# Kernel optimization log

Measured on AMD Instinct MI355X. Metric: run time of the kernel, lower is better.

## Reference

```python
import jax, jax.numpy as jnp
import numpy as np

B, N, P = 1, 8192, 2           # batch, volume points, global params
V, K = 5, 8                    # output variables, neighbor samples
H = HA = 256                   # basis hidden, aggregation hidden
DPOS = DGEO = DPAR = 256       # encoding dims
NOISE_INTENSITY = 50.0         # sampling radius = 1/noise_intensity


def setup_inputs() -> dict:
    key = jax.random.key(0)
    ks = jax.random.split(key, 18)
    s = 0.05
    return {
        "volume_mesh_centers": jax.random.normal(ks[0], (B, N, 3), jnp.float32),
        "encoding_g": jax.random.normal(ks[1], (B, N, DGEO), jnp.float32),
        "encoding_node": jax.random.normal(ks[2], (B, N, DPOS), jnp.float32),
        "global_params_values": jax.random.uniform(ks[3], (B, P, 1), jnp.float32, 0.5, 1.5),
        "global_params_reference": jnp.ones((B, P, 1), jnp.float32),
        # per-variable basis MLP (stacked over V)
        "Wb1": s * jax.random.normal(ks[4], (V, 3, H), jnp.float32),
        "bb1": s * jax.random.normal(ks[5], (V, H), jnp.float32),
        "Wb2": s * jax.random.normal(ks[6], (V, H, H), jnp.float32),
        "bb2": s * jax.random.normal(ks[7], (V, H), jnp.float32),
        # parameter model
        "Wp": s * jax.random.normal(ks[8], (P, DPAR), jnp.float32),
        "bp": s * jax.random.normal(ks[9], (DPAR,), jnp.float32),
        # per-variable aggregation MLP; first layer weight split by input block
        "Wa1_basis": s * jax.random.normal(ks[10], (V, H, HA), jnp.float32),
        "Wa1_node": s * jax.random.normal(ks[11], (V, DPOS, HA), jnp.float32),
        "Wa1_geo": s * jax.random.normal(ks[12], (V, DGEO, HA), jnp.float32),
        "Wa1_param": s * jax.random.normal(ks[13], (V, DPAR, HA), jnp.float32),
        "ba1": s * jax.random.normal(ks[14], (V, HA), jnp.float32),
        "Wa2": s * jax.random.normal(ks[15], (V, HA), jnp.float32),
        "ba2": s * jax.random.normal(ks[16], (V,), jnp.float32),
    }


def reference(volume_mesh_centers, encoding_g, encoding_node,
              global_params_values, global_params_reference,
              Wb1, bb1, Wb2, bb2, Wp, bp,
              Wa1_basis, Wa1_node, Wa1_geo, Wa1_param, ba1, Wa2, ba2):
    r = 1.0 / NOISE_INTENSITY
    b, n, _ = volume_mesh_centers.shape
    kd, kr = jax.random.split(jax.random.key(42))

    # sample_sphere: uniform-in-volume samples around each center.
    # NOTE: faithful to torch.rand_like(unsqueezed_center) -> per-coordinate radius.
    d = jax.random.normal(kd, (b, n, K, 3), volume_mesh_centers.dtype)
    d = d / jnp.linalg.norm(d, axis=-1, keepdims=True)
    radii = r * jax.random.uniform(kr, (b, n, K, 3), volume_mesh_centers.dtype) ** (1.0 / 3.0)
    samples = volume_mesh_centers[:, :, None, :] + d * radii
    # perturbed centers: original point first, then K neighbors -> (B,N,S,3)
    coords = jnp.concatenate([volume_mesh_centers[:, :, None, :], samples], axis=2)

    # parameter encoding: normalize by reference, expand over N (value is
    # identical for every point, so compute once per batch), then param MLP.
    ratio = (global_params_values / global_params_reference)[..., 0]  # (B,P)
    pe = jax.nn.relu(ratio @ Wp + bp)  # (B,DPAR)

    # per-variable basis MLP over all perturbed points: (B,N,S,V,H)
    h1 = jax.nn.relu(jnp.einsum('bnsc,vch->bnsvh', coords, Wb1) + bb1)
    h2 = jax.nn.relu(jnp.einsum('bnsvh,vhg->bnsvg', h1, Wb2) + bb2)

    # aggregation layer 1 = Linear(concat(basis, enc_node, enc_g, pe)).
    # Split the concat-matmul; encoding blocks are S-independent -> compute once.
    enc = (jnp.einsum('bnd,vdh->bnvh', encoding_node, Wa1_node)
           + jnp.einsum('bnd,vdh->bnvh', encoding_g, Wa1_geo)
           + jnp.einsum('bd,vdh->bvh', pe, Wa1_param)[:, None]
           + ba1)  # (B,N,V,HA)
    a1 = jax.nn.relu(jnp.einsum('bnsvg,vgh->bnsvh', h2, Wa1_basis) + enc[:, :, None])
    out = jnp.einsum('bnsvh,vh->bnsv', a1, Wa2) + ba2  # (B,N,S,V)

    # average: half weight on center prediction, half on mean of neighbors
    return 0.5 * out[:, :, 0] + 0.5 * jnp.mean(out[:, :, 1:], axis=2)  # (B,N,V)
```

## Files before the change

kernel.cpp:

```cpp
#include <hip/hip_runtime.h>

typedef unsigned int u32;
typedef unsigned short u16;
typedef short short8 __attribute__((ext_vector_type(8)));
typedef float f32x4 __attribute__((ext_vector_type(4)));
typedef u32 u32x2 __attribute__((ext_vector_type(2)));
typedef u32 u32x4 __attribute__((ext_vector_type(4)));

#define DEV static __device__ __forceinline__

__host__ __device__ constexpr u32 rotl32(u32 x, int r){ return (x << r) | (x >> (32 - r)); }
struct TF2 { u32 a, b; };

__host__ __device__ constexpr TF2 threefry2x32(u32 k0, u32 k1, u32 x0, u32 x1){
  u32 ks0 = k0, ks1 = k1, ks2 = k0 ^ k1 ^ 0x1BD11BDAu;
  x0 += ks0; x1 += ks1;
  x0 += x1; x1 = rotl32(x1,13); x1 ^= x0;
  x0 += x1; x1 = rotl32(x1,15); x1 ^= x0;
  x0 += x1; x1 = rotl32(x1,26); x1 ^= x0;
  x0 += x1; x1 = rotl32(x1, 6); x1 ^= x0;
  x0 += ks1; x1 += ks2 + 1u;
  x0 += x1; x1 = rotl32(x1,17); x1 ^= x0;
  x0 += x1; x1 = rotl32(x1,29); x1 ^= x0;
  x0 += x1; x1 = rotl32(x1,16); x1 ^= x0;
  x0 += x1; x1 = rotl32(x1,24); x1 ^= x0;
  x0 += ks2; x1 += ks0 + 2u;
  x0 += x1; x1 = rotl32(x1,13); x1 ^= x0;
  x0 += x1; x1 = rotl32(x1,15); x1 ^= x0;
  x0 += x1; x1 = rotl32(x1,26); x1 ^= x0;
  x0 += x1; x1 = rotl32(x1, 6); x1 ^= x0;
  x0 += ks0; x1 += ks1 + 3u;
  x0 += x1; x1 = rotl32(x1,17); x1 ^= x0;
  x0 += x1; x1 = rotl32(x1,29); x1 ^= x0;
  x0 += x1; x1 = rotl32(x1,16); x1 ^= x0;
  x0 += x1; x1 = rotl32(x1,24); x1 ^= x0;
  x0 += ks1; x1 += ks2 + 4u;
  x0 += x1; x1 = rotl32(x1,13); x1 ^= x0;
  x0 += x1; x1 = rotl32(x1,15); x1 ^= x0;
  x0 += x1; x1 = rotl32(x1,26); x1 ^= x0;
  x0 += x1; x1 = rotl32(x1, 6); x1 ^= x0;
  x0 += ks2; x1 += ks0 + 5u;
  return TF2{x0, x1};
}

DEV u32 rndbits(u32 ka, u32 kb, u32 e){
  TF2 r = threefry2x32(ka, kb, 0u, e);
  return r.a ^ r.b;
}
DEV float u01(u32 bits){
  return __builtin_bit_cast(float, (bits >> 9) | 0x3f800000u) - 1.0f;
}

DEV u32 f2bf(float f){
  u32 x = __builtin_bit_cast(u32, f);
  return (x + 0x7FFFu + ((x >> 16) & 1u)) >> 16;
}
DEV u32 pack2(float lo, float hi){ return f2bf(lo) | (f2bf(hi) << 16); }
DEV float bf2f(u32 h){ return __builtin_bit_cast(float, h << 16); }

DEV int tile32_off(int row, int k){
  return row*64 + ((((k >> 3) ^ ((row >> 1) & 3))) << 4) + ((k & 7) << 1);
}
DEV int act_off(int r, int c){
  return r*512 + ((((c >> 3) ^ (r & 7))) << 4) + ((c & 7) << 1);
}

DEV void gload16(const void* gp, void* lp){
  __builtin_amdgcn_global_load_lds(
      (const __attribute__((address_space(1))) void*)gp,
      (__attribute__((address_space(3))) void*)lp,
      16, 0, 0);
}

DEV f32x4 mfma16(short8 a, short8 b, f32x4 c){
  return __builtin_amdgcn_mfma_f32_16x16x32_bf16(a, b, c, 0, 0, 0);
}

__global__ __launch_bounds__(256) void k_wpre(
    const float* __restrict__ Wb2, const float* __restrict__ Wab,
    const float* __restrict__ Wan, const float* __restrict__ Wag,
    short8* __restrict__ wpre){
  int gid = blockIdx.x*256 + threadIdx.x;
  int v = gid >> 15;
  int rem = gid & 32767;
  short8 pk;
  if(rem < 16384){
    const float* M = (rem < 8192) ? Wb2 : Wab;
    int loc = rem & 8191;
    int kk = loc >> 10;
    int c  = (loc >> 2) & 255;
    int ku = loc & 3;
    int k0 = kk*32 + ku*8;
    #pragma unroll
    for(int j = 0; j < 8; ++j)
      pk[j] = (short)f2bf(M[(v*256 + k0 + j)*256 + c]);
  } else {
    int loc = rem - 16384;
    int kk = loc >> 10;
    int w  = loc & 1023;
    int i  = w >> 8, tt = w & 255;
    int c  = i*64 + (tt >> 2);
    int k0 = kk*32 + (((tt & 3) ^ ((c >> 1) & 3)) << 3);
    #pragma unroll
    for(int j = 0; j < 8; ++j){
      int k = k0 + j;
      float val = (k < 256) ? Wan[(v*256 + k)*256 + c]
                            : Wag[(v*256 + (k - 256))*256 + c];
      pk[j] = (short)f2bf(val);
    }
  }
  wpre[gid] = pk;
}

__global__ __launch_bounds__(256) void k_coords(
    const float* __restrict__ centers, float* __restrict__ coords){
  int q = blockIdx.x*256 + threadIdx.x;
  int n = q >> 3, k = q & 7;
  constexpr TF2 KD = threefry2x32(0u, 42u, 0u, 0u);
  constexpr TF2 KR = threefry2x32(0u, 42u, 0u, 1u);
  float d[3], uu[3];
  #pragma unroll
  for(int c = 0; c < 3; ++c){
    u32 e = (u32)(q*3 + c);
    float fd = u01(rndbits(KD.a, KD.b, e));
    float fr = u01(rndbits(KR.a, KR.b, e));
    float un = fmaxf(-0.99999994f, fd*2.0f + (-0.99999994f));
    d[c]  = 1.41421356f * erfinvf(un);
    uu[c] = fr;
  }
  float nr = sqrtf(d[0]*d[0] + d[1]*d[1] + d[2]*d[2]);
  #pragma unroll
  for(int c = 0; c < 3; ++c){
    float ctr = centers[n*3 + c];
    float val = ctr + (d[c]/nr) * (0.02f * powf(uu[c], 0.33333334f));
    coords[((k + 1)*8192 + n)*3 + c] = val;
    if(k == 0) coords[n*3 + c] = ctr;
  }
}

__global__ __launch_bounds__(256) void k_pecb(
    const float* __restrict__ gpv, const float* __restrict__ gpr,
    const float* __restrict__ Wp,  const float* __restrict__ bp,
    const float* __restrict__ Wap, const float* __restrict__ ba1,
    float* __restrict__ cb){
  __shared__ float pe[256];
  int t = threadIdx.x, v = blockIdx.x;
  float r0 = gpv[0]/gpr[0], r1 = gpv[1]/gpr[1];
  pe[t] = fmaxf(r0*Wp[t] + r1*Wp[256 + t] + bp[t], 0.f);
  __syncthreads();
  float s = ba1[v*256 + t];
  #pragma unroll 8
  for(int d = 0; d < 256; ++d) s += pe[d] * Wap[(v*256 + d)*256 + t];
  cb[v*256 + t] = s;
}

__global__ __launch_bounds__(256) void k_enc(
    const short8* __restrict__ wpre, const float* __restrict__ en,
    const float* __restrict__ eg, const float* __restrict__ cb,
    u16* __restrict__ enc){
  __shared__ __align__(16) char lds[32768];
  char* ach = lds;
  char* bch = lds + 16384;
  int bx0 = blockIdx.x;
  int bx = (bx0 & 7)*80 + (bx0 >> 3);
  int t = threadIdx.x;
  int v  = bx >> 7;
  int n0 = (bx & 127) * 64;
  int wv = t >> 6, lane = t & 63, lc = lane & 15, hi = lane >> 4;
  f32x4 acc[4][4];
  #pragma unroll
  for(int mt = 0; mt < 4; ++mt)
    #pragma unroll
    for(int nt = 0; nt < 4; ++nt) acc[mt][nt] = f32x4{0.f,0.f,0.f,0.f};
  int bsr = t >> 2, bq = t & 3;
  #pragma unroll
  for(int kk = 0; kk < 16; ++kk){
    __syncthreads();
    const short8* wsrc = wpre + (v*32768 + 16384 + kk*1024 + t);
    #pragma unroll
    for(int i = 0; i < 4; ++i) gload16(wsrc + i*256, ach + i*4096 + wv*1024);
    {
      const float* src = ((kk < 8) ? en : eg) + (n0 + bsr)*256 + (kk & 7)*32 + bq*8;
      f32x4 f0 = *(const f32x4*)(src);
      f32x4 f1 = *(const f32x4*)(src + 4);
      u32x4 w; w[0] = pack2(f0[0], f0[1]); w[1] = pack2(f0[2], f0[3]);
      w[2] = pack2(f1[0], f1[1]); w[3] = pack2(f1[2], f1[3]);
      *(u32x4*)(bch + tile32_off(bsr, bq*8)) = w;
    }
    asm volatile("s_waitcnt vmcnt(0)" ::: "memory");
    __syncthreads();
    short8 a[4], b[4];
    #pragma unroll
    for(int mt = 0; mt < 4; ++mt)
      a[mt] = *(const short8*)(ach + tile32_off(64*wv + 16*mt + lc, hi*8));
    #pragma unroll
    for(int nt = 0; nt < 4; ++nt)
      b[nt] = *(const short8*)(bch + tile32_off(16*nt + lc, hi*8));
    #pragma unroll
    for(int mt = 0; mt < 4; ++mt)
      #pragma unroll
      for(int nt = 0; nt < 4; ++nt)
        acc[mt][nt] = mfma16(a[mt], b[nt], acc[mt][nt]);
  }
  __syncthreads();
  #pragma unroll
  for(int mt = 0; mt < 4; ++mt){
    f32x4 cbv = *(const f32x4*)(cb + v*256 + 64*wv + 16*mt + 4*hi);
    #pragma unroll
    for(int nt = 0; nt < 4; ++nt){
      u32x2 pk;
      pk[0] = pack2(acc[mt][nt][0] + cbv[0], acc[mt][nt][1] + cbv[1]);
      pk[1] = pack2(acc[mt][nt][2] + cbv[2], acc[mt][nt][3] + cbv[3]);
      *(u32x2*)(lds + act_off(16*nt + lc, 64*wv + 16*mt + 4*hi)) = pk;
    }
  }
  __syncthreads();
  #pragma unroll
  for(int i = 0; i < 8; ++i){
    int L = i*256 + t; int r = L >> 5; int u = L & 31;
    u32x4 val = *(const u32x4*)(lds + act_off(r, u*8));
    *(u32x4*)(enc + (size_t)(v*8192 + n0 + r)*256 + u*8) = val;
  }
}

__global__ __launch_bounds__(256) void k_main(
    const short8* __restrict__ wpre, const float* __restrict__ coords,
    const float* __restrict__ Wb1, const float* __restrict__ bb1,
    const float* __restrict__ bb2, const u16* __restrict__ enc,
    const float* __restrict__ Wa2, float* __restrict__ part){
  __shared__ __align__(16) char act[32768];
  __shared__ float red[64][4];
  int t = threadIdx.x;
  int bx0 = blockIdx.x;
  int bx = (bx0 & 7)*720 + (bx0 >> 3);
  int v = bx / 1152; int rem = bx - v*1152;
  int s = rem >> 7; int n0 = (rem & 127)*64;
  int wv = t >> 6, lane = t & 63, lc = lane & 15, hi = lane >> 4;

  int base0 = lc*512 + 16*(hi ^ (lc & 3));
  int ks = ((lc >> 2) & 1) * 64;
  const char* bE = act + (base0 + ks);
  const char* bO = act + (base0 - ks);

  short8 a1f[4], b1f[4];
  short8 z8 = {};
  #pragma unroll
  for(int i = 0; i < 4; ++i){ a1f[i] = z8; b1f[i] = z8; }
  if(hi == 0){
    #pragma unroll
    for(int mt = 0; mt < 4; ++mt){
      int c = 64*wv + 16*mt + lc;
      float w0 = Wb1[v*768 + c], w1 = Wb1[v*768 + 256 + c], w2 = Wb1[v*768 + 512 + c];
      float bb = bb1[v*256 + c];
      u32x4 q; q[0] = pack2(w0, w1); q[1] = pack2(w2, w0);
      q[2] = pack2(w1, w2); q[3] = pack2(bb, 0.f);
      a1f[mt] = __builtin_bit_cast(short8, q);
    }
    #pragma unroll
    for(int nt = 0; nt < 4; ++nt){
      const float* cp = coords + (size_t)(s*8192 + n0 + 16*nt + lc)*3;
      float x = cp[0], y = cp[1], z = cp[2];
      float xh = bf2f(f2bf(x)), yh = bf2f(f2bf(y)), zh = bf2f(f2bf(z));
      u32x4 q;
      q[0] = pack2(x, y);
      q[1] = pack2(z, x - xh);
      q[2] = pack2(y - yh, z - zh);
      q[3] = pack2(1.0f, 0.f);
      b1f[nt] = __builtin_bit_cast(short8, q);
    }
  }

  f32x4 acc[4][4];
  #pragma unroll
  for(int mt = 0; mt < 4; ++mt)
    #pragma unroll
    for(int nt = 0; nt < 4; ++nt) acc[mt][nt] = f32x4{0.f,0.f,0.f,0.f};

  #pragma unroll
  for(int mt = 0; mt < 4; ++mt)
    #pragma unroll
    for(int nt = 0; nt < 4; ++nt)
      acc[mt][nt] = mfma16(a1f[mt], b1f[nt], acc[mt][nt]);

  auto repack = [&](const float* bias){
    #pragma unroll
    for(int mt = 0; mt < 4; ++mt){
      f32x4 bv = f32x4{0.f,0.f,0.f,0.f};
      if(bias) bv = *(const f32x4*)(bias + 64*wv + 16*mt + 4*hi);
      #pragma unroll
      for(int nt = 0; nt < 4; ++nt){
        f32x4 h = acc[mt][nt];
        u32x2 pk;
        pk[0] = pack2(fmaxf(h[0] + bv[0], 0.f), fmaxf(h[1] + bv[1], 0.f));
        pk[1] = pack2(fmaxf(h[2] + bv[2], 0.f), fmaxf(h[3] + bv[3], 0.f));
        *(u32x2*)(act + act_off(16*nt + lc, 64*wv + 16*mt + 4*hi)) = pk;
        acc[mt][nt] = f32x4{0.f,0.f,0.f,0.f};
      }
    }
  };
  repack(nullptr);
  __syncthreads();

  const char* wbytes = (const char*)wpre + (size_t)v*524288 + (size_t)((64*wv + lc)*64 + hi*16);
  auto gemm = [&](int gm){
    const char* pw = wbytes + gm*131072;
    short8 aw[2][4];
    #pragma unroll
    for(int mt = 0; mt < 4; ++mt) aw[0][mt] = *(const short8*)(pw + mt*1024);
    #pragma unroll
    for(int kk = 0; kk < 8; ++kk){
      if(kk < 7){
        #pragma unroll
        for(int mt = 0; mt < 4; ++mt)
          aw[(kk & 1) ^ 1][mt] = *(const short8*)(pw + (kk + 1)*16384 + mt*1024);
      }
      const char* bp = (kk & 1) ? bO : bE;
      short8 bfr[4];
      #pragma unroll
      for(int nt = 0; nt < 4; ++nt)
        bfr[nt] = *(const short8*)(bp + nt*8192 + kk*64);
      #pragma unroll
      for(int mt = 0; mt < 4; ++mt)
        #pragma unroll
        for(int nt = 0; nt < 4; ++nt)
          acc[mt][nt] = mfma16(aw[kk & 1][mt], bfr[nt], acc[mt][nt]);
    }
  };

  gemm(0);
  __syncthreads();
  repack(bb2 + v*256);
  __syncthreads();
  gemm(1);
  __syncthreads();

  {
    const u16* encp = enc + (size_t)(v*8192 + n0)*256;
    #pragma unroll
    for(int i = 0; i < 8; ++i){
      int r = i*8 + (t >> 5); int u = t & 31;
      u32x4 val = *(const u32x4*)(encp + (size_t)r*256 + u*8);
      *(u32x4*)(act + act_off(r, u*8)) = val;
    }
  }
  __syncthreads();

  f32x4 w4[4];
  #pragma unroll
  for(int mt = 0; mt < 4; ++mt)
    w4[mt] = *(const f32x4*)(Wa2 + v*256 + 64*wv + 16*mt + 4*hi);
  #pragma unroll
  for(int nt = 0; nt < 4; ++nt){
    float p = 0.f;
    #pragma unroll
    for(int mt = 0; mt < 4; ++mt){
      u32x2 e2 = *(const u32x2*)(act + act_off(16*nt + lc, 64*wv + 16*mt + 4*hi));
      f32x4 h = acc[mt][nt];
      float a0 = fmaxf(h[0] + bf2f(e2[0] & 0xFFFFu), 0.f);
      float a1 = fmaxf(h[1] + bf2f(e2[0] >> 16),     0.f);
      float a2 = fmaxf(h[2] + bf2f(e2[1] & 0xFFFFu), 0.f);
      float a3 = fmaxf(h[3] + bf2f(e2[1] >> 16),     0.f);
      p += a0*w4[mt][0] + a1*w4[mt][1] + a2*w4[mt][2] + a3*w4[mt][3];
    }
    p += __shfl_xor(p, 16, 64);
    p += __shfl_xor(p, 32, 64);
    if(hi == 0) red[16*nt + lc][wv] = p;
  }
  __syncthreads();
  if(t < 64){
    float sum = red[t][0] + red[t][1] + red[t][2] + red[t][3];
    part[(v*9 + s)*8192 + n0 + t] = sum;
  }
}

__global__ __launch_bounds__(256) void k_fin(
    const float* __restrict__ part, const float* __restrict__ ba2,
    float* __restrict__ out){
  int i = blockIdx.x*256 + threadIdx.x;
  if(i >= 40960) return;
  int n = i / 5, v = i - n*5;
  const float* p = part + v*73728 + n;
  float sm = 0.f;
  #pragma unroll
  for(int s = 1; s < 9; ++s) sm += p[s*8192];
  out[i] = ba2[v] + 0.5f*p[0] + 0.0625f*sm;
}

extern "C" void kernel_launch(void* const* d_in, const int* in_sizes, int n_in,
                              void* d_out, int out_size, void* d_ws, size_t ws_size,
                              hipStream_t stream){
  const float* centers = (const float*)d_in[0];
  const float* eg   = (const float*)d_in[1];
  const float* en   = (const float*)d_in[2];
  const float* gpv  = (const float*)d_in[3];
  const float* gpr  = (const float*)d_in[4];
  const float* Wb1  = (const float*)d_in[5];
  const float* bb1  = (const float*)d_in[6];
  const float* Wb2  = (const float*)d_in[7];
  const float* bb2  = (const float*)d_in[8];
  const float* Wp   = (const float*)d_in[9];
  const float* bp   = (const float*)d_in[10];
  const float* Wab  = (const float*)d_in[11];
  const float* Wan  = (const float*)d_in[12];
  const float* Wag  = (const float*)d_in[13];
  const float* Wap  = (const float*)d_in[14];
  const float* ba1  = (const float*)d_in[15];
  const float* Wa2  = (const float*)d_in[16];
  const float* ba2  = (const float*)d_in[17];
  float* out = (float*)d_out;
  char* ws = (char*)d_ws;

  short8* wpre  = (short8*)(ws);
  float* coords = (float*) (ws + 2621440);
  float* cb     = (float*) (ws + 3506176);
  float* partb  = (float*) (ws + 3511296);
  u16*   enc    = (u16*)   (ws + 4985856);

  k_wpre  <<<640,  256, 0, stream>>>(Wb2, Wab, Wan, Wag, wpre);
  k_coords<<<256,  256, 0, stream>>>(centers, coords);
  k_pecb  <<<5,    256, 0, stream>>>(gpv, gpr, Wp, bp, Wap, ba1, cb);
  k_enc   <<<640,  256, 0, stream>>>(wpre, en, eg, cb, enc);
  k_main  <<<5760, 256, 0, stream>>>(wpre, coords, Wb1, bb1, bb2, enc, Wa2, partb);
  k_fin   <<<160,  256, 0, stream>>>(partb, ba2, out);
}
```

Before: 191.5 us.

## Use hardware bf16 pack, fold biases into accumulator init, remap blocks per XCD

Replaces the software round-to-nearest bf16 packing with the v_cvt_pk_bf16_f32 instruction. Biases are now loaded once into registers and used to initialise the MFMA accumulators, so the explicit bias adds in the repack step and the bias slot in the first-layer fragments go away. The block-to-work mapping is also changed so the 9 samples of one (v, n0) tile are scheduled consecutively on the same XCD. That should let the shared encoding and weight tiles be reused from that XCD's L2. The costs are extra registers for the bias vectors and reliance on inline asm for the conversion.

Result: faster. 162.9 us (-14.9%).

```diff
diff --git a/kernel.cpp b/kernel.cpp
--- a/kernel.cpp
+++ b/kernel.cpp
@@ -55,7 +55,11 @@
   u32 x = __builtin_bit_cast(u32, f);
   return (x + 0x7FFFu + ((x >> 16) & 1u)) >> 16;
 }
-DEV u32 pack2(float lo, float hi){ return f2bf(lo) | (f2bf(hi) << 16); }
+DEV u32 pack2(float lo, float hi){
+  u32 r;
+  asm("v_cvt_pk_bf16_f32 %0, %1, %2" : "=v"(r) : "v"(lo), "v"(hi));
+  return r;
+}
 DEV float bf2f(u32 h){ return __builtin_bit_cast(float, h << 16); }
 
 DEV int tile32_off(int row, int k){
@@ -232,9 +236,13 @@
   __shared__ float red[64][4];
   int t = threadIdx.x;
   int bx0 = blockIdx.x;
-  int bx = (bx0 & 7)*720 + (bx0 >> 3);
-  int v = bx / 1152; int rem = bx - v*1152;
-  int s = rem >> 7; int n0 = (rem & 127)*64;
+  int xcd = bx0 & 7;
+  int idx = bx0 >> 3;
+  int grp = idx / 9;
+  int s   = idx - grp*9;
+  int g   = xcd*80 + grp;
+  int v   = g >> 7;
+  int n0  = (g & 127) * 64;
   int wv = t >> 6, lane = t & 63, lc = lane & 15, hi = lane >> 4;
 
   int base0 = lc*512 + 16*(hi ^ (lc & 3));
@@ -242,6 +250,13 @@
   const char* bE = act + (base0 + ks);
   const char* bO = act + (base0 - ks);
 
+  f32x4 bv1[4], bv2[4];
+  #pragma unroll
+  for(int mt = 0; mt < 4; ++mt){
+    bv1[mt] = *(const f32x4*)(bb1 + v*256 + 64*wv + 16*mt + 4*hi);
+    bv2[mt] = *(const f32x4*)(bb2 + v*256 + 64*wv + 16*mt + 4*hi);
+  }
+
   short8 a1f[4], b1f[4];
   short8 z8 = {};
   #pragma unroll
@@ -251,9 +266,8 @@
     for(int mt = 0; mt < 4; ++mt){
       int c = 64*wv + 16*mt + lc;
       float w0 = Wb1[v*768 + c], w1 = Wb1[v*768 + 256 + c], w2 = Wb1[v*768 + 512 + c];
-      float bb = bb1[v*256 + c];
       u32x4 q; q[0] = pack2(w0, w1); q[1] = pack2(w2, w0);
-      q[2] = pack2(w1, w2); q[3] = pack2(bb, 0.f);
+      q[2] = pack2(w1, w2); q[3] = 0u;
       a1f[mt] = __builtin_bit_cast(short8, q);
     }
     #pragma unroll
@@ -265,7 +279,7 @@
       q[0] = pack2(x, y);
       q[1] = pack2(z, x - xh);
       q[2] = pack2(y - yh, z - zh);
-      q[3] = pack2(1.0f, 0.f);
+      q[3] = 0u;
       b1f[nt] = __builtin_bit_cast(short8, q);
     }
   }
@@ -274,7 +288,7 @@
   #pragma unroll
   for(int mt = 0; mt < 4; ++mt)
     #pragma unroll
-    for(int nt = 0; nt < 4; ++nt) acc[mt][nt] = f32x4{0.f,0.f,0.f,0.f};
+    for(int nt = 0; nt < 4; ++nt) acc[mt][nt] = bv1[mt];
 
   #pragma unroll
   for(int mt = 0; mt < 4; ++mt)
@@ -282,23 +296,23 @@
     for(int nt = 0; nt < 4; ++nt)
       acc[mt][nt] = mfma16(a1f[mt], b1f[nt], acc[mt][nt]);
 
-  auto repack = [&](const float* bias){
-    #pragma unroll
-    for(int mt = 0; mt < 4; ++mt){
-      f32x4 bv = f32x4{0.f,0.f,0.f,0.f};
-      if(bias) bv = *(const f32x4*)(bias + 64*wv + 16*mt + 4*hi);
+  auto repack = [&](){
+    #pragma unroll
+    for(int mt = 0; mt < 4; ++mt)
       #pragma unroll
       for(int nt = 0; nt < 4; ++nt){
         f32x4 h = acc[mt][nt];
         u32x2 pk;
-        pk[0] = pack2(fmaxf(h[0] + bv[0], 0.f), fmaxf(h[1] + bv[1], 0.f));
-        pk[1] = pack2(fmaxf(h[2] + bv[2], 0.f), fmaxf(h[3] + bv[3], 0.f));
+        pk[0] = pack2(fmaxf(h[0], 0.f), fmaxf(h[1], 0.f));
+        pk[1] = pack2(fmaxf(h[2], 0.f), fmaxf(h[3], 0.f));
         *(u32x2*)(act + act_off(16*nt + lc, 64*wv + 16*mt + 4*hi)) = pk;
-        acc[mt][nt] = f32x4{0.f,0.f,0.f,0.f};
       }
-    }
   };
-  repack(nullptr);
+  repack();
+  #pragma unroll
+  for(int mt = 0; mt < 4; ++mt)
+    #pragma unroll
+    for(int nt = 0; nt < 4; ++nt) acc[mt][nt] = bv2[mt];
   __syncthreads();
 
   const char* wbytes = (const char*)wpre + (size_t)v*524288 + (size_t)((64*wv + lc)*64 + hi*16);
@@ -329,7 +343,11 @@
 
   gemm(0);
   __syncthreads();
-  repack(bb2 + v*256);
+  repack();
+  #pragma unroll
+  for(int mt = 0; mt < 4; ++mt)
+    #pragma unroll
+    for(int nt = 0; nt < 4; ++nt) acc[mt][nt] = f32x4{0.f,0.f,0.f,0.f};
   __syncthreads();
   gemm(1);
   __syncthreads();
```
